# Kernel optimization log

Hardware: AMD Instinct MI355X
Metric: run time of the kernel (lower is better)

Reference implementation:

```python
import jax, jax.numpy as jnp
import numpy as np
import math

D_MODEL = 1024
NUM_NEURONS = 2048
LUT_SIZE = 4096
TWO_PI = 2.0 * math.pi


def lut_sin_cos(theta, sin_table, cos_table):
    # Interpolated periodic table lookup over [0, 2*pi)
    n = sin_table.shape[0]
    pos = (theta / TWO_PI) * n
    pos = jnp.mod(pos, n)
    i0 = jnp.floor(pos).astype(jnp.int32)
    frac = pos - i0.astype(theta.dtype)
    i1 = jnp.mod(i0 + 1, n)
    s = sin_table[i0] * (1.0 - frac) + sin_table[i1] * frac
    c = cos_table[i0] * (1.0 - frac) + cos_table[i1] * frac
    return s, c


def setup_inputs() -> dict:
    key = jax.random.key(0)
    ks = jax.random.split(key, 10)
    B = 64
    x_real = jax.random.normal(ks[0], (B, D_MODEL), jnp.float32)
    x_imag = jax.random.normal(ks[1], (B, D_MODEL), jnp.float32)
    t = jax.random.uniform(ks[2], (B,), jnp.float32)
    # xavier_uniform with gain=0.5 for linear weights
    def xavier(k, shape, gain):
        fan_out, fan_in = shape
        a = gain * math.sqrt(6.0 / (fan_in + fan_out))
        return jax.random.uniform(k, shape, jnp.float32, -a, a)
    ic_w = xavier(ks[3], (D_MODEL, 2 * D_MODEL), 0.5)
    ic_b = jnp.zeros((D_MODEL,), jnp.float32)
    W = jax.random.normal(ks[4], (NUM_NEURONS, D_MODEL), jnp.float32) * 0.02
    Bp = jnp.zeros((NUM_NEURONS, D_MODEL), jnp.float32)
    attn_cos = jnp.ones((NUM_NEURONS, D_MODEL), jnp.float32)
    attn_sin = jnp.ones((NUM_NEURONS, D_MODEL), jnp.float32)
    wr = xavier(ks[5], (D_MODEL, NUM_NEURONS), 0.5)
    wi = xavier(ks[6], (D_MODEL, NUM_NEURONS), 0.5)
    grid = jnp.arange(LUT_SIZE, dtype=jnp.float32) * (TWO_PI / LUT_SIZE)
    sin_table = jnp.sin(grid)
    cos_table = jnp.cos(grid)
    return {"x_real": x_real, "x_imag": x_imag, "t": t,
            "ic_w": ic_w, "ic_b": ic_b, "W": W, "Bp": Bp,
            "attn_cos": attn_cos, "attn_sin": attn_sin,
            "wr": wr, "wi": wi,
            "sin_table": sin_table, "cos_table": cos_table}


def reference(x_real, x_imag, t, ic_w, ic_b, W, Bp, attn_cos, attn_sin, wr, wi, sin_table, cos_table):
    x_combined = jnp.concatenate([x_real, x_imag], axis=-1)          # [B, 2D]
    x_collapsed = x_combined @ ic_w.T + ic_b                          # [B, D]
    wavelength = 1.0 + jnp.abs(W)                                     # [N, D]
    theta = x_collapsed[:, None, :] / wavelength + Bp + t[:, None, None]  # [B, N, D]
    sin_t, cos_t = lut_sin_cos(theta, sin_table, cos_table)
    cos_sum = jnp.einsum('bnd,nd->bn', cos_t, attn_cos)               # fused weight+reduce
    sin_sum = jnp.einsum('bnd,nd->bn', sin_t, attn_sin)
    out_real = jax.nn.silu(cos_sum @ wr.T)                            # [B, D]
    out_imag = jax.nn.silu(sin_sum @ wi.T)
    return out_real, out_imag
```

## Files before the change

kernel.cpp:

```cpp
#include <hip/hip_runtime.h>
#include <stdint.h>

#define DM 1024
#define NN 2048
#define BB 64

static constexpr float INV2PI = 0.15915494309189535f;

__device__ __forceinline__ uint32_t bf16r(float x) {
  uint32_t b = __float_as_uint(x);
  b += 0x7fffu + ((b >> 16) & 1u);
  return b >> 16;
}

__global__ __launch_bounds__(256) void k0_prep(
    const float* __restrict__ xr, const float* __restrict__ xi,
    const float* __restrict__ W,
    float* __restrict__ xcombP, float* __restrict__ rinv)
{
  __shared__ float tile[64][65];
  int bid = blockIdx.x;
  int t = threadIdx.x;
  if (bid < 32) {
    int j = bid;
    int k0 = j * 64;
    const float* src = (k0 < 1024) ? xr : xi;
    int koff = k0 & 1023;
    int c = t & 63, rl = t >> 6;
#pragma unroll
    for (int i = 0; i < 16; ++i) {
      int b = rl * 16 + i;
      tile[b][c] = src[b * 1024 + koff + c];
    }
    __syncthreads();
    float2* out2 = (float2*)xcombP;
    int bl = t & 63, kp = t >> 6;
#pragma unroll
    for (int i = 0; i < 8; ++i) {
      int kl = (kp * 8 + i) * 2;
      float2 v = make_float2(tile[bl][kl], tile[bl][kl + 1]);
      out2[(size_t)((k0 + kl) >> 1) * 64 + bl] = v;
    }
  } else {
    int j = bid - 32;
    const float4* W4 = (const float4*)W;
    float4* R4 = (float4*)rinv;
    int base = j * 2048 + t;
#pragma unroll
    for (int i = 0; i < 8; ++i) {
      int idx = base + i * 256;
      float4 w = W4[idx];
      float4 r;
      r.x = 1.0f / (1.0f + fabsf(w.x));
      r.y = 1.0f / (1.0f + fabsf(w.y));
      r.z = 1.0f / (1.0f + fabsf(w.z));
      r.w = 1.0f / (1.0f + fabsf(w.w));
      R4[idx] = r;
    }
  }
}

__global__ __launch_bounds__(512) void k1_collapse(
    const float* __restrict__ xcombP, const float* __restrict__ icw,
    const float* __restrict__ icb, uint32_t* __restrict__ xcp)
{
  __shared__ float part[8][4][64];
  int d0 = blockIdx.x * 4;
  int wave = __builtin_amdgcn_readfirstlane((int)(threadIdx.x >> 6));
  int lane = threadIdx.x & 63;
  const float2* P2 = (const float2*)xcombP;
  float acc[4] = {0.f, 0.f, 0.f, 0.f};
  int kbase = wave * 256;
  for (int kk = 0; kk < 256; kk += 4) {
    int k = kbase + kk;
    float2 xa = P2[(size_t)(k >> 1) * 64 + lane];
    float2 xb = P2[(size_t)((k >> 1) + 1) * 64 + lane];
#pragma unroll
    for (int r = 0; r < 4; ++r) {
      float4 w = *(const float4*)(icw + (size_t)(d0 + r) * 2048 + k);
      acc[r] = fmaf(w.x, xa.x, acc[r]);
      acc[r] = fmaf(w.y, xa.y, acc[r]);
      acc[r] = fmaf(w.z, xb.x, acc[r]);
      acc[r] = fmaf(w.w, xb.y, acc[r]);
    }
  }
#pragma unroll
  for (int r = 0; r < 4; ++r) part[wave][r][lane] = acc[r];
  __syncthreads();
  int t = threadIdx.x;
  if (t < 128) {
    int pj = t >> 6;
    int b = t & 63;
    float s0 = 0.f, s1 = 0.f;
#pragma unroll
    for (int w = 0; w < 8; ++w) {
      s0 += part[w][2 * pj][b];
      s1 += part[w][2 * pj + 1][b];
    }
    float x0 = (s0 + icb[d0 + 2 * pj]) * INV2PI;
    float x1 = (s1 + icb[d0 + 2 * pj + 1]) * INV2PI;
    uint32_t u = bf16r(x0) | (bf16r(x1) << 16);
    xcp[(size_t)((d0 >> 1) + pj) * 64 + b] = u;
  }
}

#define K2_STEP(r4, b4, a4, s4, xu0, xu1)                                 \
  do {                                                                     \
    float x0 = __uint_as_float((xu0) << 16);                               \
    float x1 = __uint_as_float((xu0) & 0xffff0000u);                       \
    float x2 = __uint_as_float((xu1) << 16);                               \
    float x3 = __uint_as_float((xu1) & 0xffff0000u);                       \
    float rv0 = fmaf(x0, (r4).x, fmaf((b4).x, INV2PI, t2));                \
    accc0 = fmaf(__builtin_amdgcn_cosf(rv0), (a4).x, accc0);               \
    accs0 = fmaf(__builtin_amdgcn_sinf(rv0), (s4).x, accs0);               \
    float rv1 = fmaf(x1, (r4).y, fmaf((b4).y, INV2PI, t2));                \
    accc1 = fmaf(__builtin_amdgcn_cosf(rv1), (a4).y, accc1);               \
    accs1 = fmaf(__builtin_amdgcn_sinf(rv1), (s4).y, accs1);               \
    float rv2 = fmaf(x2, (r4).z, fmaf((b4).z, INV2PI, t2));                \
    accc0 = fmaf(__builtin_amdgcn_cosf(rv2), (a4).z, accc0);               \
    accs0 = fmaf(__builtin_amdgcn_sinf(rv2), (s4).z, accs0);               \
    float rv3 = fmaf(x3, (r4).w, fmaf((b4).w, INV2PI, t2));                \
    accc1 = fmaf(__builtin_amdgcn_cosf(rv3), (a4).w, accc1);               \
    accs1 = fmaf(__builtin_amdgcn_sinf(rv3), (s4).w, accs1);               \
  } while (0)

__global__ __launch_bounds__(512) void k2_resonant(
    const uint32_t* __restrict__ xcp, const float* __restrict__ rinv,
    const float* __restrict__ Bp, const float* __restrict__ ac,
    const float* __restrict__ as_, const float* __restrict__ tin,
    float* __restrict__ csP, float* __restrict__ ssP)
{
  __shared__ __align__(16) float lds[2][8][4][64];
  int wave = __builtin_amdgcn_readfirstlane((int)(threadIdx.x >> 6));
  int lane = threadIdx.x & 63;
  int bid = blockIdx.x;
  int q = bid & 3;
  int n = (bid >> 2) * 8 + wave;
  float t2 = tin[lane] * INV2PI;

  int g = lane >> 4;
  const float* ab = (g == 0) ? rinv : (g == 1) ? Bp : (g == 2) ? ac : as_;
  const float* gp = ab + (size_t)n * 1024 + (size_t)q * 256 + (lane & 15) * 4;

  const uint32_t* xp = xcp + (size_t)(q * 128) * 64 + lane;

  __builtin_amdgcn_global_load_lds(
      (const __attribute__((address_space(1))) void*)gp,
      (__attribute__((address_space(3))) void*)&lds[0][wave][0][0], 16, 0, 0);
  uint32_t xu0 = xp[0], xu1 = xp[64];

  float accc0 = 0.f, accs0 = 0.f, accc1 = 0.f, accs1 = 0.f;

#pragma unroll
  for (int c = 0; c < 4; ++c) {
    if (c < 3) {
      __builtin_amdgcn_global_load_lds(
          (const __attribute__((address_space(1))) void*)(gp + (c + 1) * 64),
          (__attribute__((address_space(3))) void*)&lds[(c + 1) & 1][wave][0][0],
          16, 0, 0);
      asm volatile("s_waitcnt vmcnt(1)" ::: "memory");
    } else {
      asm volatile("s_waitcnt vmcnt(0)" ::: "memory");
    }
    const float4* pr = (const float4*)&lds[c & 1][wave][0][0];
#pragma unroll 4
    for (int i = 0; i < 16; ++i) {
      int ga = c * 16 + i;
      uint32_t cu0 = xu0, cu1 = xu1;
      xu0 = xp[(size_t)(2 * ga + 2) * 64];
      xu1 = xp[(size_t)(2 * ga + 3) * 64];
      float4 r4 = pr[i];
      float4 b4 = pr[16 + i];
      float4 a4 = pr[32 + i];
      float4 s4 = pr[48 + i];
      K2_STEP(r4, b4, a4, s4, cu0, cu1);
    }
  }

  size_t o = ((size_t)q * 2048 + n) * 64 + lane;
  csP[o] = accc0 + accc1;
  ssP[o] = accs0 + accs1;
}

__global__ __launch_bounds__(256) void k2b_reduce(
    const float* __restrict__ csP, const float* __restrict__ ssP,
    float* __restrict__ csT, float* __restrict__ ssT)
{
  int i = blockIdx.x * 256 + threadIdx.x;
  float c = csP[i] + csP[i + 131072] + csP[i + 262144] + csP[i + 393216];
  float s = ssP[i] + ssP[i + 131072] + ssP[i + 262144] + ssP[i + 393216];
  csT[i] = c;
  ssT[i] = s;
}

__global__ __launch_bounds__(512) void k3_out(
    const float* __restrict__ csT, const float* __restrict__ ssT,
    const float* __restrict__ wr, const float* __restrict__ wi,
    float* __restrict__ out)
{
  __shared__ float part[8][4][65];
  int bid = blockIdx.x;
  int sel = bid >> 8;
  int d0 = (bid & 255) * 4;
  int wave = __builtin_amdgcn_readfirstlane((int)(threadIdx.x >> 6));
  int lane = threadIdx.x & 63;
  const float* src = sel ? ssT : csT;
  const float* wt = sel ? wi : wr;
  float acc[4] = {0.f, 0.f, 0.f, 0.f};
  int n0 = wave * 256;
  for (int i = 0; i < 64; ++i) {
    int n = n0 + i * 4;
    float cv0 = src[(size_t)(n + 0) * 64 + lane];
    float cv1 = src[(size_t)(n + 1) * 64 + lane];
    float cv2 = src[(size_t)(n + 2) * 64 + lane];
    float cv3 = src[(size_t)(n + 3) * 64 + lane];
#pragma unroll
    for (int r = 0; r < 4; ++r) {
      float4 wv = *(const float4*)(wt + (size_t)(d0 + r) * 2048 + n);
      acc[r] = fmaf(cv0, wv.x, acc[r]);
      acc[r] = fmaf(cv1, wv.y, acc[r]);
      acc[r] = fmaf(cv2, wv.z, acc[r]);
      acc[r] = fmaf(cv3, wv.w, acc[r]);
    }
  }
#pragma unroll
  for (int r = 0; r < 4; ++r) part[wave][r][lane] = acc[r];
  __syncthreads();
  int t = threadIdx.x;
  if (t < 256) {
    int b = t >> 2, j = t & 3;
    float s = 0.f;
#pragma unroll
    for (int w = 0; w < 8; ++w) s += part[w][j][b];
    float y = s / (1.0f + __expf(-s));
    out[(size_t)sel * 65536 + (size_t)b * 1024 + d0 + j] = y;
  }
}

extern "C" void kernel_launch(void* const* d_in, const int* in_sizes, int n_in,
                              void* d_out, int out_size, void* d_ws, size_t ws_size,
                              hipStream_t stream) {
  const float* xr  = (const float*)d_in[0];
  const float* xi  = (const float*)d_in[1];
  const float* t   = (const float*)d_in[2];
  const float* icw = (const float*)d_in[3];
  const float* icb = (const float*)d_in[4];
  const float* W   = (const float*)d_in[5];
  const float* Bp  = (const float*)d_in[6];
  const float* ac  = (const float*)d_in[7];
  const float* as_ = (const float*)d_in[8];
  const float* wr  = (const float*)d_in[9];
  const float* wi  = (const float*)d_in[10];

  float* ws = (float*)d_ws;
  float* rinv   = ws;
  float* xcombP = ws + 2097152;
  uint32_t* xcp = (uint32_t*)(ws + 2228224);
  float* csP    = ws + 2260992;
  float* ssP    = ws + 2785280;
  float* csT    = ws + 3309568;
  float* ssT    = ws + 3440640;
  float* out = (float*)d_out;

  k0_prep<<<dim3(288), dim3(256), 0, stream>>>(xr, xi, W, xcombP, rinv);
  k1_collapse<<<dim3(256), dim3(512), 0, stream>>>(xcombP, icw, icb, xcp);
  k2_resonant<<<dim3(1024), dim3(512), 0, stream>>>(xcp, rinv, Bp, ac, as_, t, csP, ssP);
  k2b_reduce<<<dim3(512), dim3(256), 0, stream>>>(csP, ssP, csT, ssT);
  k3_out<<<dim3(512), dim3(512), 0, stream>>>(csT, ssT, wr, wi, out);
}
```

Before: 80.72 us.

## Stage collapsed activations in LDS and double GEMV grid with register prefetch

The resonant kernel now loads its quarter of the bf16-packed collapsed activations into LDS once per block with async global-to-LDS copies, replacing per-iteration global loads by each wave. The collapse and output GEMV kernels each handle two output rows per block instead of four, which doubles their grid size, and they prefetch the next activation vector in registers. The aim is to raise occupancy and parallelism on the small GEMVs and to cut redundant global traffic in the main kernel. The costs are an added block barrier, extra LDS use, and less reuse of each activation load across output rows.

```diff
diff --git a/kernel.cpp b/kernel.cpp
--- a/kernel.cpp
+++ b/kernel.cpp
@@ -64,43 +64,48 @@
     const float* __restrict__ xcombP, const float* __restrict__ icw,
     const float* __restrict__ icb, uint32_t* __restrict__ xcp)
 {
-  __shared__ float part[8][4][64];
-  int d0 = blockIdx.x * 4;
+  __shared__ float part[8][2][64];
+  int d0 = blockIdx.x * 2;
   int wave = __builtin_amdgcn_readfirstlane((int)(threadIdx.x >> 6));
   int lane = threadIdx.x & 63;
   const float2* P2 = (const float2*)xcombP;
-  float acc[4] = {0.f, 0.f, 0.f, 0.f};
+  float acc0 = 0.f, acc1 = 0.f;
   int kbase = wave * 256;
+  float2 xa = P2[(size_t)(kbase >> 1) * 64 + lane];
+  float2 xb = P2[(size_t)((kbase >> 1) + 1) * 64 + lane];
   for (int kk = 0; kk < 256; kk += 4) {
     int k = kbase + kk;
-    float2 xa = P2[(size_t)(k >> 1) * 64 + lane];
-    float2 xb = P2[(size_t)((k >> 1) + 1) * 64 + lane];
-#pragma unroll
-    for (int r = 0; r < 4; ++r) {
-      float4 w = *(const float4*)(icw + (size_t)(d0 + r) * 2048 + k);
-      acc[r] = fmaf(w.x, xa.x, acc[r]);
-      acc[r] = fmaf(w.y, xa.y, acc[r]);
-      acc[r] = fmaf(w.z, xb.x, acc[r]);
-      acc[r] = fmaf(w.w, xb.y, acc[r]);
-    }
-  }
-#pragma unroll
-  for (int r = 0; r < 4; ++r) part[wave][r][lane] = acc[r];
+    int kn = (kk < 252) ? (k + 4) : kbase;
+    float2 na = P2[(size_t)(kn >> 1) * 64 + lane];
+    float2 nb = P2[(size_t)((kn >> 1) + 1) * 64 + lane];
+    float4 w0 = *(const float4*)(icw + (size_t)d0 * 2048 + k);
+    float4 w1 = *(const float4*)(icw + (size_t)(d0 + 1) * 2048 + k);
+    acc0 = fmaf(w0.x, xa.x, acc0);
+    acc0 = fmaf(w0.y, xa.y, acc0);
+    acc0 = fmaf(w0.z, xb.x, acc0);
+    acc0 = fmaf(w0.w, xb.y, acc0);
+    acc1 = fmaf(w1.x, xa.x, acc1);
+    acc1 = fmaf(w1.y, xa.y, acc1);
+    acc1 = fmaf(w1.z, xb.x, acc1);
+    acc1 = fmaf(w1.w, xb.y, acc1);
+    xa = na; xb = nb;
+  }
+  part[wave][0][lane] = acc0;
+  part[wave][1][lane] = acc1;
   __syncthreads();
   int t = threadIdx.x;
-  if (t < 128) {
-    int pj = t >> 6;
-    int b = t & 63;
+  if (t < 64) {
+    int b = t;
     float s0 = 0.f, s1 = 0.f;
 #pragma unroll
     for (int w = 0; w < 8; ++w) {
-      s0 += part[w][2 * pj][b];
-      s1 += part[w][2 * pj + 1][b];
-    }
-    float x0 = (s0 + icb[d0 + 2 * pj]) * INV2PI;
-    float x1 = (s1 + icb[d0 + 2 * pj + 1]) * INV2PI;
+      s0 += part[w][0][b];
+      s1 += part[w][1][b];
+    }
+    float x0 = (s0 + icb[d0]) * INV2PI;
+    float x1 = (s1 + icb[d0 + 1]) * INV2PI;
     uint32_t u = bf16r(x0) | (bf16r(x1) << 16);
-    xcp[(size_t)((d0 >> 1) + pj) * 64 + b] = u;
+    xcp[(size_t)(d0 >> 1) * 64 + b] = u;
   }
 }
 
@@ -130,7 +135,8 @@
     const float* __restrict__ as_, const float* __restrict__ tin,
     float* __restrict__ csP, float* __restrict__ ssP)
 {
-  __shared__ __align__(16) float lds[2][8][4][64];
+  __shared__ __align__(16) uint32_t xlds[128][64];
+  __shared__ __align__(16) float plds[2][8][4][64];
   int wave = __builtin_amdgcn_readfirstlane((int)(threadIdx.x >> 6));
   int lane = threadIdx.x & 63;
   int bid = blockIdx.x;
@@ -138,16 +144,24 @@
   int n = (bid >> 2) * 8 + wave;
   float t2 = tin[lane] * INV2PI;
 
+  const char* xsrc = (const char*)(xcp + (size_t)q * 128 * 64);
+  char* xdst = (char*)&xlds[0][0];
+#pragma unroll
+  for (int r = 0; r < 4; ++r) {
+    int j = wave * 4 + r;
+    __builtin_amdgcn_global_load_lds(
+        (const __attribute__((address_space(1))) void*)(xsrc + j * 1024 + lane * 16),
+        (__attribute__((address_space(3))) void*)(xdst + j * 1024), 16, 0, 0);
+  }
+
   int g = lane >> 4;
   const float* ab = (g == 0) ? rinv : (g == 1) ? Bp : (g == 2) ? ac : as_;
   const float* gp = ab + (size_t)n * 1024 + (size_t)q * 256 + (lane & 15) * 4;
-
-  const uint32_t* xp = xcp + (size_t)(q * 128) * 64 + lane;
-
   __builtin_amdgcn_global_load_lds(
       (const __attribute__((address_space(1))) void*)gp,
-      (__attribute__((address_space(3))) void*)&lds[0][wave][0][0], 16, 0, 0);
-  uint32_t xu0 = xp[0], xu1 = xp[64];
+      (__attribute__((address_space(3))) void*)&plds[0][wave][0][0], 16, 0, 0);
+
+  __syncthreads();
 
   float accc0 = 0.f, accs0 = 0.f, accc1 = 0.f, accs1 = 0.f;
 
@@ -156,24 +170,23 @@
     if (c < 3) {
       __builtin_amdgcn_global_load_lds(
           (const __attribute__((address_space(1))) void*)(gp + (c + 1) * 64),
-          (__attribute__((address_space(3))) void*)&lds[(c + 1) & 1][wave][0][0],
+          (__attribute__((address_space(3))) void*)&plds[(c + 1) & 1][wave][0][0],
           16, 0, 0);
       asm volatile("s_waitcnt vmcnt(1)" ::: "memory");
     } else {
       asm volatile("s_waitcnt vmcnt(0)" ::: "memory");
     }
-    const float4* pr = (const float4*)&lds[c & 1][wave][0][0];
+    const float4* pr = (const float4*)&plds[c & 1][wave][0][0];
 #pragma unroll 4
     for (int i = 0; i < 16; ++i) {
       int ga = c * 16 + i;
-      uint32_t cu0 = xu0, cu1 = xu1;
-      xu0 = xp[(size_t)(2 * ga + 2) * 64];
-      xu1 = xp[(size_t)(2 * ga + 3) * 64];
+      uint32_t xu0 = xlds[2 * ga][lane];
+      uint32_t xu1 = xlds[2 * ga + 1][lane];
       float4 r4 = pr[i];
       float4 b4 = pr[16 + i];
       float4 a4 = pr[32 + i];
       float4 s4 = pr[48 + i];
-      K2_STEP(r4, b4, a4, s4, cu0, cu1);
+      K2_STEP(r4, b4, a4, s4, xu0, xu1);
     }
   }
 
@@ -198,37 +211,45 @@
     const float* __restrict__ wr, const float* __restrict__ wi,
     float* __restrict__ out)
 {
-  __shared__ float part[8][4][65];
+  __shared__ float part[8][2][64];
   int bid = blockIdx.x;
-  int sel = bid >> 8;
-  int d0 = (bid & 255) * 4;
+  int sel = bid >> 9;
+  int d0 = (bid & 511) * 2;
   int wave = __builtin_amdgcn_readfirstlane((int)(threadIdx.x >> 6));
   int lane = threadIdx.x & 63;
   const float* src = sel ? ssT : csT;
   const float* wt = sel ? wi : wr;
-  float acc[4] = {0.f, 0.f, 0.f, 0.f};
+  float acc0 = 0.f, acc1 = 0.f;
   int n0 = wave * 256;
+  float cv0 = src[(size_t)(n0 + 0) * 64 + lane];
+  float cv1 = src[(size_t)(n0 + 1) * 64 + lane];
+  float cv2 = src[(size_t)(n0 + 2) * 64 + lane];
+  float cv3 = src[(size_t)(n0 + 3) * 64 + lane];
   for (int i = 0; i < 64; ++i) {
     int n = n0 + i * 4;
-    float cv0 = src[(size_t)(n + 0) * 64 + lane];
-    float cv1 = src[(size_t)(n + 1) * 64 + lane];
-    float cv2 = src[(size_t)(n + 2) * 64 + lane];
-    float cv3 = src[(size_t)(n + 3) * 64 + lane];
-#pragma unroll
-    for (int r = 0; r < 4; ++r) {
-      float4 wv = *(const float4*)(wt + (size_t)(d0 + r) * 2048 + n);
-      acc[r] = fmaf(cv0, wv.x, acc[r]);
-      acc[r] = fmaf(cv1, wv.y, acc[r]);
-      acc[r] = fmaf(cv2, wv.z, acc[r]);
-      acc[r] = fmaf(cv3, wv.w, acc[r]);
-    }
-  }
-#pragma unroll
-  for (int r = 0; r < 4; ++r) part[wave][r][lane] = acc[r];
+    int nn = (i < 63) ? (n + 4) : n0;
+    float nv0 = src[(size_t)(nn + 0) * 64 + lane];
+    float nv1 = src[(size_t)(nn + 1) * 64 + lane];
+    float nv2 = src[(size_t)(nn + 2) * 64 + lane];
+    float nv3 = src[(size_t)(nn + 3) * 64 + lane];
+    float4 w0 = *(const float4*)(wt + (size_t)d0 * 2048 + n);
+    float4 w1 = *(const float4*)(wt + (size_t)(d0 + 1) * 2048 + n);
+    acc0 = fmaf(cv0, w0.x, acc0);
+    acc0 = fmaf(cv1, w0.y, acc0);
+    acc0 = fmaf(cv2, w0.z, acc0);
+    acc0 = fmaf(cv3, w0.w, acc0);
+    acc1 = fmaf(cv0, w1.x, acc1);
+    acc1 = fmaf(cv1, w1.y, acc1);
+    acc1 = fmaf(cv2, w1.z, acc1);
+    acc1 = fmaf(cv3, w1.w, acc1);
+    cv0 = nv0; cv1 = nv1; cv2 = nv2; cv3 = nv3;
+  }
+  part[wave][0][lane] = acc0;
+  part[wave][1][lane] = acc1;
   __syncthreads();
   int t = threadIdx.x;
-  if (t < 256) {
-    int b = t >> 2, j = t & 3;
+  if (t < 128) {
+    int b = t >> 1, j = t & 1;
     float s = 0.f;
 #pragma unroll
     for (int w = 0; w < 8; ++w) s += part[w][j][b];
@@ -263,8 +284,8 @@
   float* out = (float*)d_out;
 
   k0_prep<<<dim3(288), dim3(256), 0, stream>>>(xr, xi, W, xcombP, rinv);
-  k1_collapse<<<dim3(256), dim3(512), 0, stream>>>(xcombP, icw, icb, xcp);
+  k1_collapse<<<dim3(512), dim3(512), 0, stream>>>(xcombP, icw, icb, xcp);
   k2_resonant<<<dim3(1024), dim3(512), 0, stream>>>(xcp, rinv, Bp, ac, as_, t, csP, ssP);
   k2b_reduce<<<dim3(512), dim3(256), 0, stream>>>(csP, ssP, csT, ssT);
-  k3_out<<<dim3(512), dim3(512), 0, stream>>>(csT, ssT, wr, wi, out);
-}
+  k3_out<<<dim3(1024), dim3(512), 0, stream>>>(csT, ssT, wr, wi, out);
+}
```

New measurement: 91.64 us. 1.14x slower.

## Stage collapsed x tile in LDS and split resonant D into eight chunks

Applied to the files above, without the earlier changes.

The resonant kernel now splits the D dimension into 8 chunks of 128 instead of 4 of 256, which doubles the grid to 2048 blocks. Each block cooperatively loads its x tile into LDS once, and all 8 waves read it from there instead of issuing per-lane global loads. The per-neuron parameter chunks are loaded up front and followed by a block barrier, which drops the per-wave double-buffered pipeline. The partial buffers double in size and the reduce kernel sums 8 partials, so there is more partial traffic and less overlap within a block.

```diff
diff --git a/kernel.cpp b/kernel.cpp
--- a/kernel.cpp
+++ b/kernel.cpp
@@ -130,50 +130,52 @@
     const float* __restrict__ as_, const float* __restrict__ tin,
     float* __restrict__ csP, float* __restrict__ ssP)
 {
-  __shared__ __align__(16) float lds[2][8][4][64];
+  __shared__ __align__(16) uint32_t xlds[64][64];
+  __shared__ __align__(16) float plds[2][8][4][64];
   int wave = __builtin_amdgcn_readfirstlane((int)(threadIdx.x >> 6));
   int lane = threadIdx.x & 63;
   int bid = blockIdx.x;
-  int q = bid & 3;
-  int n = (bid >> 2) * 8 + wave;
+  int q = bid & 7;
+  int n = (bid >> 3) * 8 + wave;
   float t2 = tin[lane] * INV2PI;
+
+  const char* xsrc = (const char*)(xcp + (size_t)q * 64 * 64);
+  char* xdst = (char*)&xlds[0][0];
+#pragma unroll
+  for (int r = 0; r < 2; ++r) {
+    int j = wave * 2 + r;
+    __builtin_amdgcn_global_load_lds(
+        (const __attribute__((address_space(1))) void*)(xsrc + j * 1024 + lane * 16),
+        (__attribute__((address_space(3))) void*)(xdst + j * 1024), 16, 0, 0);
+  }
 
   int g = lane >> 4;
   const float* ab = (g == 0) ? rinv : (g == 1) ? Bp : (g == 2) ? ac : as_;
-  const float* gp = ab + (size_t)n * 1024 + (size_t)q * 256 + (lane & 15) * 4;
-
-  const uint32_t* xp = xcp + (size_t)(q * 128) * 64 + lane;
-
-  __builtin_amdgcn_global_load_lds(
-      (const __attribute__((address_space(1))) void*)gp,
-      (__attribute__((address_space(3))) void*)&lds[0][wave][0][0], 16, 0, 0);
-  uint32_t xu0 = xp[0], xu1 = xp[64];
+  const float* gp = ab + (size_t)n * 1024 + (size_t)q * 128 + (lane & 15) * 4;
+#pragma unroll
+  for (int c = 0; c < 2; ++c) {
+    __builtin_amdgcn_global_load_lds(
+        (const __attribute__((address_space(1))) void*)(gp + c * 64),
+        (__attribute__((address_space(3))) void*)&plds[c][wave][0][0], 16, 0, 0);
+  }
+
+  __syncthreads();
 
   float accc0 = 0.f, accs0 = 0.f, accc1 = 0.f, accs1 = 0.f;
 
 #pragma unroll
-  for (int c = 0; c < 4; ++c) {
-    if (c < 3) {
-      __builtin_amdgcn_global_load_lds(
-          (const __attribute__((address_space(1))) void*)(gp + (c + 1) * 64),
-          (__attribute__((address_space(3))) void*)&lds[(c + 1) & 1][wave][0][0],
-          16, 0, 0);
-      asm volatile("s_waitcnt vmcnt(1)" ::: "memory");
-    } else {
-      asm volatile("s_waitcnt vmcnt(0)" ::: "memory");
-    }
-    const float4* pr = (const float4*)&lds[c & 1][wave][0][0];
+  for (int c = 0; c < 2; ++c) {
+    const float4* pr = (const float4*)&plds[c][wave][0][0];
 #pragma unroll 4
     for (int i = 0; i < 16; ++i) {
       int ga = c * 16 + i;
-      uint32_t cu0 = xu0, cu1 = xu1;
-      xu0 = xp[(size_t)(2 * ga + 2) * 64];
-      xu1 = xp[(size_t)(2 * ga + 3) * 64];
+      uint32_t xu0 = xlds[2 * ga][lane];
+      uint32_t xu1 = xlds[2 * ga + 1][lane];
       float4 r4 = pr[i];
       float4 b4 = pr[16 + i];
       float4 a4 = pr[32 + i];
       float4 s4 = pr[48 + i];
-      K2_STEP(r4, b4, a4, s4, cu0, cu1);
+      K2_STEP(r4, b4, a4, s4, xu0, xu1);
     }
   }
 
@@ -187,8 +189,12 @@
     float* __restrict__ csT, float* __restrict__ ssT)
 {
   int i = blockIdx.x * 256 + threadIdx.x;
-  float c = csP[i] + csP[i + 131072] + csP[i + 262144] + csP[i + 393216];
-  float s = ssP[i] + ssP[i + 131072] + ssP[i + 262144] + ssP[i + 393216];
+  float c = 0.f, s = 0.f;
+#pragma unroll
+  for (int j = 0; j < 8; ++j) {
+    c += csP[i + j * 131072];
+    s += ssP[i + j * 131072];
+  }
   csT[i] = c;
   ssT[i] = s;
 }
@@ -257,14 +263,14 @@
   float* xcombP = ws + 2097152;
   uint32_t* xcp = (uint32_t*)(ws + 2228224);
   float* csP    = ws + 2260992;
-  float* ssP    = ws + 2785280;
-  float* csT    = ws + 3309568;
-  float* ssT    = ws + 3440640;
+  float* ssP    = ws + 3309568;
+  float* csT    = ws + 4358144;
+  float* ssT    = ws + 4489216;
   float* out = (float*)d_out;
 
   k0_prep<<<dim3(288), dim3(256), 0, stream>>>(xr, xi, W, xcombP, rinv);
   k1_collapse<<<dim3(256), dim3(512), 0, stream>>>(xcombP, icw, icb, xcp);
-  k2_resonant<<<dim3(1024), dim3(512), 0, stream>>>(xcp, rinv, Bp, ac, as_, t, csP, ssP);
+  k2_resonant<<<dim3(2048), dim3(512), 0, stream>>>(xcp, rinv, Bp, ac, as_, t, csP, ssP);
   k2b_reduce<<<dim3(512), dim3(256), 0, stream>>>(csP, ssP, csT, ssT);
   k3_out<<<dim3(512), dim3(512), 0, stream>>>(csT, ssT, wr, wi, out);
 }
```

Measured after the change: 78.20 us. 3.1% less time.
